# Performance work log

Measured on AMD Instinct MI355X. Metric: run time of the kernel, lower is better.

Reference implementation:

```python
import jax, jax.numpy as jnp
import numpy as np
import math

B, C, F, W = 2, 8, 512, 1024
HEADS = 8


def _mcl(x, Wm, b):
    # per-channel linear over feature dim: x (b,c,g,w), Wm (c,f,g), b (c,f)
    return jnp.einsum('bcgw,cfg->bcfw', x, Wm) + b[None, :, :, None]


def _conv(x, w, b, pad):
    y = jax.lax.conv_general_dilated(
        x, w, window_strides=(1, 1), padding=[(0, 0), (pad, pad)],
        dimension_numbers=('NCHW', 'OIHW', 'NCHW'))
    return y + b[None, :, None, None]


def _rope(t):
    # t: (..., seq, d); lucidrains-style interleaved rotary
    d = t.shape[-1]
    seq = t.shape[-2]
    inv_freq = 1.0 / (10000.0 ** (jnp.arange(0, d, 2, dtype=jnp.float32) / d))
    freqs = jnp.arange(seq, dtype=jnp.float32)[:, None] * inv_freq[None, :]  # (seq, d/2)
    emb = jnp.repeat(freqs, 2, axis=-1)  # (seq, d), interleaved f0,f0,f1,f1,...
    cos, sin = jnp.cos(emb), jnp.sin(emb)
    tp = t.reshape(t.shape[:-1] + (d // 2, 2))
    rot = jnp.stack([-tp[..., 1], tp[..., 0]], axis=-1).reshape(t.shape)
    return t * cos.astype(t.dtype) + rot * sin.astype(t.dtype)


def setup_inputs() -> dict:
    key = jax.random.key(0)
    ks = jax.random.split(key, 18)
    s = 0.02
    d = {'x': jax.random.normal(ks[0], (B, C, F, W), dtype=jnp.float32)}
    names = ['q', 'k', 'v', 'o']
    for i, n in enumerate(names):
        d['W' + n] = jax.random.normal(ks[1 + 4 * i], (C, F, F), dtype=jnp.float32) * s
        d['b' + n] = jnp.zeros((C, F), dtype=jnp.float32)
        kw = 7 if n != 'o' else 1
        d[n + '_conv_w'] = jax.random.normal(ks[2 + 4 * i], (C, C, 1, kw), dtype=jnp.float32) * s
        d[n + '_conv_b'] = jnp.zeros((C,), dtype=jnp.float32)
    return d


def reference(x, Wq, bq, q_conv_w, q_conv_b, Wk, bk, k_conv_w, k_conv_b,
              Wv, bv, v_conv_w, v_conv_b, Wo, bo, o_conv_w, o_conv_b):
    b, c, h, w = x.shape
    dh = h // HEADS

    def split_heads(y):  # (b,c,h,w) -> (b,c,heads,w,dh)
        return y.transpose(0, 1, 3, 2).reshape(b, c, w, HEADS, dh).transpose(0, 1, 3, 2, 4)

    q = _rope(split_heads(_conv(_mcl(x, Wq, bq), q_conv_w, q_conv_b, 3)))
    k = _rope(split_heads(_conv(_mcl(x, Wk, bk), k_conv_w, k_conv_b, 3)))
    v = split_heads(_conv(_mcl(x, Wv, bv), v_conv_w, v_conv_b, 3))

    # forced fp32 attention, scaled by sqrt(h) = sqrt(features)
    qk = jnp.einsum('bceqd,bcekd->bceqk', q.astype(jnp.float32), k.astype(jnp.float32)) / math.sqrt(h)
    a = jax.nn.softmax(qk, axis=-1)
    o = jnp.einsum('bceqk,bcekd->bceqd', a, v.astype(jnp.float32))  # (b,c,heads,w,dh)
    o = o.transpose(0, 1, 3, 2, 4).reshape(b, c, w, h).transpose(0, 1, 3, 2)  # (b,c,h,w)

    return _conv(_mcl(o, Wo, bo), o_conv_w, o_conv_b, 0)
```

## Files before the change

kernel.cpp:

```cpp
#include <hip/hip_runtime.h>
#include <hip/hip_bf16.h>
#include <math.h>

#define W_ 1024
#define F_ 512
#define C_ 8
#define B_ 2
#define DH_ 64

typedef __attribute__((ext_vector_type(8))) short short8;
typedef __attribute__((ext_vector_type(4))) short short4v;
typedef __attribute__((ext_vector_type(4))) float f32x4;

__device__ inline unsigned short f2bf(float x) {
    union { float f; unsigned u; } v; v.f = x;
    unsigned r = v.u + 0x7fff + ((v.u >> 16) & 1);
    return (unsigned short)(r >> 16);
}

__device__ inline void gll16(const void* g, void* l) {
    __builtin_amdgcn_global_load_lds(
        (const __attribute__((address_space(1))) unsigned int*)g,
        (__attribute__((address_space(3))) unsigned int*)l, 16, 0, 0);
}

__global__ __launch_bounds__(256) void rope_table_kernel(float* __restrict__ cost,
                                                         float* __restrict__ sint) {
    int idx = blockIdx.x * 256 + threadIdx.x;
    if (idx >= W_ * 32) return;
    int w = idx >> 5, i = idx & 31;
    double freq = pow(10000.0, -(double)(2 * i) / 64.0);
    double ang = (double)w * freq;
    cost[idx] = (float)cos(ang);
    sint[idx] = (float)sin(ang);
}

__global__ __launch_bounds__(256) void xt_kernel(
    const float* __restrict__ In, unsigned short* __restrict__ Out)
{
    const int wt = blockIdx.x;
    const int gc = blockIdx.y;
    const int bc = blockIdx.z;
    __shared__ unsigned short T[128][72];
    const int t = threadIdx.x;
    const float* src = In + (size_t)bc * F_ * W_ + (size_t)gc * 64 * W_ + wt * 128;
    const int d0 = (t >> 4) * 4;
    const int w0 = (t & 15) * 4;
    #pragma unroll
    for (int it = 0; it < 2; ++it) {
        int wbase = w0 + it * 64;
        float4 row[4];
        #pragma unroll
        for (int k = 0; k < 4; ++k)
            row[k] = *(const float4*)(src + (size_t)(d0 + k) * W_ + wbase);
        #pragma unroll
        for (int wp = 0; wp < 4; ++wp) {
            ushort4 p;
            p.x = f2bf(((const float*)&row[0])[wp]);
            p.y = f2bf(((const float*)&row[1])[wp]);
            p.z = f2bf(((const float*)&row[2])[wp]);
            p.w = f2bf(((const float*)&row[3])[wp]);
            *(ushort4*)&T[wbase + wp][d0] = p;
        }
    }
    __syncthreads();
    unsigned short* dst = Out + (size_t)bc * W_ * F_ + (size_t)(wt * 128) * F_ + gc * 64;
    const int w = t >> 1, hf = (t & 1) * 32;
    const unsigned short* sr = &T[w][hf];
    uint4* dr = (uint4*)(dst + (size_t)w * F_ + hf);
    dr[0] = ((const uint4*)sr)[0];
    dr[1] = ((const uint4*)sr)[1];
    dr[2] = ((const uint4*)sr)[2];
    dr[3] = ((const uint4*)sr)[3];
}

__device__ inline void mcl_body(const unsigned short* Ag, const unsigned short* Bg,
                                const float* biasp, float* Cp,
                                int f0, int w0)
{
    __shared__ unsigned short As_[128 * 64];
    __shared__ unsigned short Bs_[128 * 64];
    __shared__ float scr[4][16 * 17];

    const int t = threadIdx.x;
    const int wid = t >> 6, lane = t & 63;
    const int l15 = lane & 15, l4 = lane >> 4;
    const int wf = wid >> 1, ww = wid & 1;

    const int grow = lane >> 3;
    const int gcol = ((lane & 7) * 16) ^ ((grow & 7) << 4);

    f32x4 acc[4][4];
    #pragma unroll
    for (int mt = 0; mt < 4; ++mt)
        #pragma unroll
        for (int nt = 0; nt < 4; ++nt) acc[mt][nt] = (f32x4){0.f, 0.f, 0.f, 0.f};

    for (int ks = 0; ks < 8; ++ks) {
        const int k0 = ks * 64;
        __syncthreads();
        #pragma unroll
        for (int i = 0; i < 4; ++i) {
            int rbase = wid * 32 + i * 8;
            int row = rbase + grow;
            gll16(Ag + (size_t)(f0 + row) * F_ + k0 + (gcol >> 1), &As_[rbase * 64]);
            gll16(Bg + (size_t)(w0 + row) * F_ + k0 + (gcol >> 1), &Bs_[rbase * 64]);
        }
        __syncthreads();
        #pragma unroll
        for (int kf = 0; kf < 2; ++kf) {
            short8 af[4], bf_[4];
            #pragma unroll
            for (int mt = 0; mt < 4; ++mt) {
                int row = wf * 64 + mt * 16 + l15;
                int off = (kf * 64 + l4 * 16) ^ ((row & 7) << 4);
                af[mt] = *(const short8*)((const char*)As_ + row * 128 + off);
            }
            #pragma unroll
            for (int nt = 0; nt < 4; ++nt) {
                int row = ww * 64 + nt * 16 + l15;
                int off = (kf * 64 + l4 * 16) ^ ((row & 7) << 4);
                bf_[nt] = *(const short8*)((const char*)Bs_ + row * 128 + off);
            }
            #pragma unroll
            for (int mt = 0; mt < 4; ++mt)
                #pragma unroll
                for (int nt = 0; nt < 4; ++nt)
                    acc[mt][nt] = __builtin_amdgcn_mfma_f32_16x16x32_bf16(af[mt], bf_[nt], acc[mt][nt], 0, 0, 0);
        }
    }

    const float* bp = biasp + f0 + wf * 64;
    float bz[4][4];
    #pragma unroll
    for (int mt = 0; mt < 4; ++mt)
        #pragma unroll
        for (int r = 0; r < 4; ++r) bz[mt][r] = bp[mt * 16 + l4 * 4 + r];

    float* sw = scr[wid];
    #pragma unroll
    for (int mt = 0; mt < 4; ++mt)
        #pragma unroll
        for (int nt = 0; nt < 4; ++nt) {
            #pragma unroll
            for (int r = 0; r < 4; ++r)
                sw[(l4 * 4 + r) * 17 + l15] = acc[mt][nt][r] + bz[mt][r];
            float4 o;
            o.x = sw[l15 * 17 + l4 * 4 + 0];
            o.y = sw[l15 * 17 + l4 * 4 + 1];
            o.z = sw[l15 * 17 + l4 * 4 + 2];
            o.w = sw[l15 * 17 + l4 * 4 + 3];
            *(float4*)(Cp + (size_t)(f0 + wf * 64 + mt * 16 + l15) * W_
                          + w0 + ww * 64 + nt * 16 + l4 * 4) = o;
        }
}

__global__ __launch_bounds__(256) void mcl_qkv_kernel(
    const unsigned short* __restrict__ Xt,
    const unsigned short* __restrict__ W0, const unsigned short* __restrict__ W1,
    const unsigned short* __restrict__ W2,
    const float* __restrict__ b0, const float* __restrict__ b1, const float* __restrict__ b2,
    float* __restrict__ Y0, float* __restrict__ Y1, float* __restrict__ Y2)
{
    const int zz = blockIdx.z;
    const int proj = zz >> 4, bc = zz & 15;
    const int c = bc & 7;
    const unsigned short* Wb = proj == 0 ? W0 : (proj == 1 ? W1 : W2);
    const float* bias = proj == 0 ? b0 : (proj == 1 ? b1 : b2);
    float* Y = proj == 0 ? Y0 : (proj == 1 ? Y1 : Y2);
    mcl_body(Wb + (size_t)c * F_ * F_, Xt + (size_t)bc * W_ * F_,
             bias + c * F_, Y + (size_t)bc * F_ * W_,
             blockIdx.y * 128, blockIdx.x * 128);
}

__global__ __launch_bounds__(256) void mcl_mfma_kernel(
    const unsigned short* __restrict__ Xt, const unsigned short* __restrict__ Wb,
    const float* __restrict__ bias, float* __restrict__ Y)
{
    const int bc = blockIdx.z;
    const int c = bc & 7;
    mcl_body(Wb + (size_t)c * F_ * F_, Xt + (size_t)bc * W_ * F_,
             bias + c * F_, Y + (size_t)bc * F_ * W_,
             blockIdx.y * 128, blockIdx.x * 128);
}

__global__ __launch_bounds__(256) void convrope3_kernel(
    float* __restrict__ Aq, float* __restrict__ Ak, float* __restrict__ Av,
    const float* __restrict__ cwq, const float* __restrict__ cbq,
    const float* __restrict__ cwk, const float* __restrict__ cbk,
    const float* __restrict__ cwv, const float* __restrict__ cbv,
    const float* __restrict__ cost, const float* __restrict__ sint)
{
    const int fp = blockIdx.x;
    const int b = blockIdx.y;
    const int proj = blockIdx.z;
    float* Y = proj == 0 ? Aq : (proj == 1 ? Ak : Av);
    const float* CW = proj == 0 ? cwq : (proj == 1 ? cwk : cwv);
    const float* CB = proj == 0 ? cbq : (proj == 1 ? cbk : cbv);
    const int do_rope = (proj < 2);

    __shared__ float rows[C_][2][W_];
    __shared__ float wT[C_][7][C_];
    const int t = threadIdx.x;

    #pragma unroll
    for (int r = 0; r < 16; r++) {
        int ci = r >> 1, fi = r & 1;
        const float* src = Y + ((size_t)(b * C_ + ci) * F_ + 2 * fp + fi) * W_;
        *(float4*)&rows[ci][fi][t * 4] = *(const float4*)(src + t * 4);
    }
    for (int idx = t; idx < C_ * C_ * 7; idx += 256) {
        int co = idx & 7; int tmp = idx >> 3; int tt = tmp % 7; int ci = tmp / 7;
        wT[ci][tt][co] = CW[((size_t)co * C_ + ci) * 7 + tt];
    }
    float cb[8];
    #pragma unroll
    for (int co = 0; co < 8; co++) cb[co] = CB[co];
    __syncthreads();

    float acc[4][2][8];
    #pragma unroll
    for (int rep = 0; rep < 4; rep++)
        #pragma unroll
        for (int fi = 0; fi < 2; fi++)
            #pragma unroll
            for (int co = 0; co < 8; co++) acc[rep][fi][co] = cb[co];

    for (int ci = 0; ci < 8; ci++) {
        #pragma unroll
        for (int tt = 0; tt < 7; tt++) {
            float wv[8];
            *(float4*)(wv)     = *(const float4*)&wT[ci][tt][0];
            *(float4*)(wv + 4) = *(const float4*)&wT[ci][tt][4];
            #pragma unroll
            for (int rep = 0; rep < 4; rep++) {
                int ws = t + rep * 256 + tt - 3;
                float v0 = 0.f, v1 = 0.f;
                if ((unsigned)ws < (unsigned)W_) { v0 = rows[ci][0][ws]; v1 = rows[ci][1][ws]; }
                #pragma unroll
                for (int co = 0; co < 8; co++) {
                    acc[rep][0][co] = fmaf(v0, wv[co], acc[rep][0][co]);
                    acc[rep][1][co] = fmaf(v1, wv[co], acc[rep][1][co]);
                }
            }
        }
    }
    const int ip = fp & 31;
    #pragma unroll
    for (int rep = 0; rep < 4; rep++) {
        int w = t + rep * 256;
        float c_ = 1.f, s_ = 0.f;
        if (do_rope) { c_ = cost[w * 32 + ip]; s_ = sint[w * 32 + ip]; }
        #pragma unroll
        for (int co = 0; co < 8; co++) {
            float o0 = acc[rep][0][co], o1 = acc[rep][1][co];
            float r0 = do_rope ? (o0 * c_ - o1 * s_) : o0;
            float r1 = do_rope ? (o1 * c_ + o0 * s_) : o1;
            size_t rowb = ((size_t)(b * C_ + co) * F_ + 2 * fp) * W_;
            Y[rowb + w] = r0;
            Y[rowb + W_ + w] = r1;
        }
    }
}

__global__ __launch_bounds__(256) void transpose_qk_kernel(
    const float* __restrict__ In, unsigned short* __restrict__ Out, float scale)
{
    const int wt = blockIdx.x;
    const int h = blockIdx.y;
    __shared__ unsigned short T[128][72];
    const int t = threadIdx.x;
    const float* src = In + (size_t)h * 64 * 1024 + wt * 128;
    const int d0 = (t >> 4) * 4;
    const int w0 = (t & 15) * 4;
    #pragma unroll
    for (int it = 0; it < 2; ++it) {
        int wbase = w0 + it * 64;
        float4 row[4];
        #pragma unroll
        for (int k = 0; k < 4; ++k)
            row[k] = *(const float4*)(src + (size_t)(d0 + k) * 1024 + wbase);
        #pragma unroll
        for (int wp = 0; wp < 4; ++wp) {
            ushort4 p;
            p.x = f2bf(((const float*)&row[0])[wp] * scale);
            p.y = f2bf(((const float*)&row[1])[wp] * scale);
            p.z = f2bf(((const float*)&row[2])[wp] * scale);
            p.w = f2bf(((const float*)&row[3])[wp] * scale);
            *(ushort4*)&T[wbase + wp][d0] = p;
        }
    }
    __syncthreads();
    unsigned short* dst = Out + ((size_t)h * 1024 + wt * 128) * 64;
    const int w = t >> 1, hf = (t & 1) * 32;
    const unsigned short* sr = &T[w][hf];
    uint4* dr = (uint4*)(dst + w * 64 + hf);
    dr[0] = ((const uint4*)sr)[0];
    dr[1] = ((const uint4*)sr)[1];
    dr[2] = ((const uint4*)sr)[2];
    dr[3] = ((const uint4*)sr)[3];
}

__global__ __launch_bounds__(256) void bf16cvt_kernel(
    const float* __restrict__ In, unsigned short* __restrict__ Out)
{
    size_t i = ((size_t)blockIdx.x * 256 + threadIdx.x) * 8;
    float4 a = *(const float4*)(In + i);
    float4 b = *(const float4*)(In + i + 4);
    ushort4 pa, pb;
    pa.x = f2bf(a.x); pa.y = f2bf(a.y); pa.z = f2bf(a.z); pa.w = f2bf(a.w);
    pb.x = f2bf(b.x); pb.y = f2bf(b.y); pb.z = f2bf(b.z); pb.w = f2bf(b.w);
    *(ushort4*)(Out + i) = pa;
    *(ushort4*)(Out + i + 4) = pb;
}

__global__ __launch_bounds__(256) void attn_mfma_kernel(
    const unsigned short* __restrict__ Qt, const unsigned short* __restrict__ Kt,
    const unsigned short* __restrict__ Vb, unsigned short* __restrict__ Ot)
{
    const int head = blockIdx.x;
    const int qt = blockIdx.y;
    const int t = threadIdx.x;
    const int wid = t >> 6;
    const int lane = t & 63;
    const int l15 = lane & 15;
    const int l4 = lane >> 4;

    __shared__ unsigned short Ks[64 * 64];
    __shared__ unsigned short Vs[64 * 64];
    __shared__ char plds_[4][11264];
    unsigned short* plds = (unsigned short*)plds_[wid];
    float* olds = (float*)plds_[wid];

    const int q0 = qt * 256 + wid * 64;
    const unsigned short* qb = Qt + ((size_t)head * 1024 + q0) * 64;
    const unsigned short* kb = Kt + (size_t)head * 1024 * 64;
    const unsigned short* vb = Vb + (size_t)head * 64 * 1024;

    short8 aq[4][2];
    #pragma unroll
    for (int mt = 0; mt < 4; ++mt)
        #pragma unroll
        for (int kf = 0; kf < 2; ++kf)
            aq[mt][kf] = *(const short8*)(qb + (size_t)(mt * 16 + l15) * 64 + kf * 32 + l4 * 8);

    const int srow = lane >> 3;
    const int schunk = lane & 7;

    f32x4 oa[4][4];
    float li[4] = {0.f, 0.f, 0.f, 0.f};
    #pragma unroll
    for (int mt = 0; mt < 4; ++mt)
        #pragma unroll
        for (int dt = 0; dt < 4; ++dt) oa[mt][dt] = (f32x4){0.f, 0.f, 0.f, 0.f};

    for (int jt = 0; jt < 16; ++jt) {
        const int j0 = jt * 64;
        __syncthreads();
        #pragma unroll
        for (int i = 0; i < 2; ++i) {
            int rbase = wid * 16 + i * 8;
            int row = rbase + srow;
            gll16(kb + (size_t)(j0 + row) * 64 + ((schunk ^ (row & 7)) * 8), &Ks[rbase * 64]);
            gll16(vb + (size_t)row * 1024 + j0 + ((schunk ^ (row & 7)) * 8), &Vs[rbase * 64]);
        }
        __syncthreads();

        #pragma unroll
        for (int nt = 0; nt < 4; ++nt) {
            int row = nt * 16 + l15;
            short8 bk0 = *(const short8*)&Ks[row * 64 + ((l4 ^ (row & 7)) * 8)];
            short8 bk1 = *(const short8*)&Ks[row * 64 + (((4 + l4) ^ (row & 7)) * 8)];
            #pragma unroll
            for (int mt = 0; mt < 4; ++mt) {
                f32x4 a0 = (f32x4){0.f, 0.f, 0.f, 0.f};
                a0 = __builtin_amdgcn_mfma_f32_16x16x32_bf16(bk0, aq[mt][0], a0, 0, 0, 0);
                a0 = __builtin_amdgcn_mfma_f32_16x16x32_bf16(bk1, aq[mt][1], a0, 0, 0, 0);
                float p0 = __builtin_exp2f(a0[0]);
                float p1 = __builtin_exp2f(a0[1]);
                float p2 = __builtin_exp2f(a0[2]);
                float p3 = __builtin_exp2f(a0[3]);
                li[mt] += (p0 + p1) + (p2 + p3);
                union { __hip_bfloat162 h2[2]; short4v s4; } pk;
                pk.h2[0] = __float22bfloat162_rn(make_float2(p0, p1));
                pk.h2[1] = __float22bfloat162_rn(make_float2(p2, p3));
                *(short4v*)(plds + (size_t)(mt * 16 + l15) * 88 + nt * 16 + l4 * 4) = pk.s4;
            }
        }
        short8 pa[4][2];
        #pragma unroll
        for (int mt = 0; mt < 4; ++mt)
            #pragma unroll
            for (int kf = 0; kf < 2; ++kf)
                pa[mt][kf] = *(const short8*)(plds + (size_t)(mt * 16 + l15) * 88 + kf * 32 + l4 * 8);
        #pragma unroll
        for (int dt = 0; dt < 4; ++dt) {
            int row = dt * 16 + l15;
            short8 bv0 = *(const short8*)&Vs[row * 64 + ((l4 ^ (row & 7)) * 8)];
            short8 bv1 = *(const short8*)&Vs[row * 64 + (((4 + l4) ^ (row & 7)) * 8)];
            #pragma unroll
            for (int mt = 0; mt < 4; ++mt) {
                oa[mt][dt] = __builtin_amdgcn_mfma_f32_16x16x32_bf16(pa[mt][0], bv0, oa[mt][dt], 0, 0, 0);
                oa[mt][dt] = __builtin_amdgcn_mfma_f32_16x16x32_bf16(pa[mt][1], bv1, oa[mt][dt], 0, 0, 0);
            }
        }
    }

    float invq[4][4];
    #pragma unroll
    for (int mt = 0; mt < 4; ++mt) {
        float l = li[mt];
        l += __shfl_xor(l, 16);
        l += __shfl_xor(l, 32);
        float inv = 1.f / l;
        #pragma unroll
        for (int r = 0; r < 4; ++r)
            invq[mt][r] = __shfl(inv, l4 * 4 + r);
    }

    #pragma unroll
    for (int mt = 0; mt < 4; ++mt) {
        #pragma unroll
        for (int dt = 0; dt < 4; ++dt)
            #pragma unroll
            for (int r = 0; r < 4; ++r)
                olds[(size_t)(l4 * 4 + r) * 68 + dt * 16 + l15] = oa[mt][dt][r] * invq[mt][r];
        const int ql = lane >> 2, hf = (lane & 3) * 16;
        const float* srow_ = olds + (size_t)ql * 68 + hf;
        unsigned short* dst = Ot + ((size_t)(head >> 3) * W_ + q0 + mt * 16 + ql) * F_
                                 + (head & 7) * 64 + hf;
        short8 pk0, pk1;
        #pragma unroll
        for (int e = 0; e < 8; ++e) { pk0[e] = (short)f2bf(srow_[e]); pk1[e] = (short)f2bf(srow_[8 + e]); }
        *(short8*)(dst) = pk0;
        *(short8*)(dst + 8) = pk1;
    }
}

__global__ __launch_bounds__(256) void oconv_kernel(
    const float* __restrict__ In, const float* __restrict__ OW,
    const float* __restrict__ OB, float* __restrict__ Out)
{
    size_t idx = (size_t)blockIdx.x * 256 + threadIdx.x;
    int b = (int)(idx >> 19);
    size_t fw = idx & (((size_t)1 << 19) - 1);
    const float* in = In + (size_t)b * C_ * F_ * W_ + fw;
    float* out = Out + (size_t)b * C_ * F_ * W_ + fw;
    float v[8];
    #pragma unroll
    for (int ci = 0; ci < 8; ci++) v[ci] = in[(size_t)ci * F_ * W_];
    #pragma unroll
    for (int co = 0; co < 8; co++) {
        float acc = OB[co];
        #pragma unroll
        for (int ci = 0; ci < 8; ci++) acc = fmaf(v[ci], OW[co * 8 + ci], acc);
        out[(size_t)co * F_ * W_] = acc;
    }
}

extern "C" void kernel_launch(void* const* d_in, const int* in_sizes, int n_in,
                              void* d_out, int out_size, void* d_ws, size_t ws_size,
                              hipStream_t stream) {
    const float* x   = (const float*)d_in[0];
    const float* Wq  = (const float*)d_in[1];
    const float* bq  = (const float*)d_in[2];
    const float* qcw = (const float*)d_in[3];
    const float* qcb = (const float*)d_in[4];
    const float* Wk  = (const float*)d_in[5];
    const float* bk  = (const float*)d_in[6];
    const float* kcw = (const float*)d_in[7];
    const float* kcb = (const float*)d_in[8];
    const float* Wv  = (const float*)d_in[9];
    const float* bv  = (const float*)d_in[10];
    const float* vcw = (const float*)d_in[11];
    const float* vcb = (const float*)d_in[12];
    const float* Wo  = (const float*)d_in[13];
    const float* bo  = (const float*)d_in[14];
    const float* ocw = (const float*)d_in[15];
    const float* ocb = (const float*)d_in[16];

    float* ws = (float*)d_ws;
    const size_t SZ = (size_t)B_ * C_ * F_ * W_;
    const size_t WSF = (size_t)C_ * F_ * F_ / 2;
    float* Aq = ws;
    float* Ak = ws + SZ;
    float* Av = ws + 2 * SZ;
    unsigned short* XtVb = (unsigned short*)(ws + 3 * SZ);
    unsigned short* WqB = (unsigned short*)(ws + 3 * SZ + SZ / 2);
    unsigned short* WkB = (unsigned short*)(ws + 3 * SZ + SZ / 2 + 2 * WSF);
    unsigned short* WvB = (unsigned short*)(ws + 3 * SZ + SZ / 2 + 4 * WSF);
    unsigned short* WoB = (unsigned short*)(ws + 3 * SZ + SZ / 2 + 6 * WSF);
    unsigned short* Qt  = (unsigned short*)(ws + 2 * SZ);
    unsigned short* Kt  = Qt + SZ;
    unsigned short* Ot  = (unsigned short*)ws;
    float* cost = ws + 4 * SZ;
    float* sint = cost + (size_t)W_ * 32;

    const float qscale = (float)(1.4426950408889634 / 22.627416997969522);

    rope_table_kernel<<<(W_ * 32 + 255) / 256, 256, 0, stream>>>(cost, sint);
    xt_kernel<<<dim3(8, 8, 16), 256, 0, stream>>>(x, XtVb);
    bf16cvt_kernel<<<1024, 256, 0, stream>>>(Wq, WqB);
    bf16cvt_kernel<<<1024, 256, 0, stream>>>(Wk, WkB);
    bf16cvt_kernel<<<1024, 256, 0, stream>>>(Wv, WvB);
    bf16cvt_kernel<<<1024, 256, 0, stream>>>(Wo, WoB);

    mcl_qkv_kernel<<<dim3(8, 4, 48), 256, 0, stream>>>(
        XtVb, WqB, WkB, WvB, bq, bk, bv, Aq, Ak, Av);

    convrope3_kernel<<<dim3(F_ / 2, B_, 3), 256, 0, stream>>>(
        Aq, Ak, Av, qcw, qcb, kcw, kcb, vcw, vcb, cost, sint);

    bf16cvt_kernel<<<SZ / (256 * 8), 256, 0, stream>>>(Av, XtVb);
    transpose_qk_kernel<<<dim3(W_ / 128, 128), 256, 0, stream>>>(Aq, Qt, qscale);
    transpose_qk_kernel<<<dim3(W_ / 128, 128), 256, 0, stream>>>(Ak, Kt, 1.0f);

    attn_mfma_kernel<<<dim3(128, 4), 256, 0, stream>>>(Qt, Kt, XtVb, Ot);

    mcl_mfma_kernel<<<dim3(8, 4, 16), 256, 0, stream>>>(Ot, WoB, bo, Ak);
    oconv_kernel<<<(B_ * F_ * W_) / 256, 256, 0, stream>>>(Ak, ocw, ocb, (float*)d_out);
}
```

Baseline: 286.6 us.

## Split conv+rope by W chunks, out-of-place, fuse V bf16 conversion

```diff
diff --git a/kernel.cpp b/kernel.cpp
--- a/kernel.cpp
+++ b/kernel.cpp
@@ -184,30 +184,30 @@
              blockIdx.y * 128, blockIdx.x * 128);
 }
 
-__global__ __launch_bounds__(256) void convrope3_kernel(
-    float* __restrict__ Aq, float* __restrict__ Ak, float* __restrict__ Av,
-    const float* __restrict__ cwq, const float* __restrict__ cbq,
-    const float* __restrict__ cwk, const float* __restrict__ cbk,
-    const float* __restrict__ cwv, const float* __restrict__ cbv,
-    const float* __restrict__ cost, const float* __restrict__ sint)
-{
-    const int fp = blockIdx.x;
-    const int b = blockIdx.y;
-    const int proj = blockIdx.z;
-    float* Y = proj == 0 ? Aq : (proj == 1 ? Ak : Av);
-    const float* CW = proj == 0 ? cwq : (proj == 1 ? cwk : cwv);
-    const float* CB = proj == 0 ? cbq : (proj == 1 ? cbk : cbv);
-    const int do_rope = (proj < 2);
-
-    __shared__ float rows[C_][2][W_];
+__global__ __launch_bounds__(256) void convrope_w_kernel(
+    const float* __restrict__ In, const float* __restrict__ CW,
+    const float* __restrict__ CB, const float* __restrict__ cost,
+    const float* __restrict__ sint, float* __restrict__ OutF,
+    unsigned short* __restrict__ OutB, int do_rope, int out_bf16)
+{
+    const int wc = blockIdx.x;
+    const int fp = blockIdx.y;
+    const int b = blockIdx.z;
+    __shared__ float rows[C_][2][264];
     __shared__ float wT[C_][7][C_];
     const int t = threadIdx.x;
-
-    #pragma unroll
-    for (int r = 0; r < 16; r++) {
+    const int w0 = wc * 256;
+
+    #pragma unroll
+    for (int r = 0; r < 16; ++r) {
         int ci = r >> 1, fi = r & 1;
-        const float* src = Y + ((size_t)(b * C_ + ci) * F_ + 2 * fp + fi) * W_;
-        *(float4*)&rows[ci][fi][t * 4] = *(const float4*)(src + t * 4);
+        const float* src = In + ((size_t)(b * C_ + ci) * F_ + 2 * fp + fi) * W_;
+        int gw = w0 + t - 3;
+        rows[ci][fi][t] = ((unsigned)gw < (unsigned)W_) ? src[gw] : 0.f;
+        if (t < 8) {
+            int gw2 = w0 + 256 + t - 3;
+            rows[ci][fi][256 + t] = ((unsigned)gw2 < (unsigned)W_) ? src[gw2] : 0.f;
+        }
     }
     for (int idx = t; idx < C_ * C_ * 7; idx += 256) {
         int co = idx & 7; int tmp = idx >> 3; int tt = tmp % 7; int ci = tmp / 7;
@@ -218,47 +218,44 @@
     for (int co = 0; co < 8; co++) cb[co] = CB[co];
     __syncthreads();
 
-    float acc[4][2][8];
-    #pragma unroll
-    for (int rep = 0; rep < 4; rep++)
-        #pragma unroll
-        for (int fi = 0; fi < 2; fi++)
-            #pragma unroll
-            for (int co = 0; co < 8; co++) acc[rep][fi][co] = cb[co];
-
-    for (int ci = 0; ci < 8; ci++) {
-        #pragma unroll
-        for (int tt = 0; tt < 7; tt++) {
+    float acc[2][8];
+    #pragma unroll
+    for (int fi = 0; fi < 2; ++fi)
+        #pragma unroll
+        for (int co = 0; co < 8; ++co) acc[fi][co] = cb[co];
+
+    for (int ci = 0; ci < 8; ++ci) {
+        #pragma unroll
+        for (int tt = 0; tt < 7; ++tt) {
             float wv[8];
             *(float4*)(wv)     = *(const float4*)&wT[ci][tt][0];
             *(float4*)(wv + 4) = *(const float4*)&wT[ci][tt][4];
-            #pragma unroll
-            for (int rep = 0; rep < 4; rep++) {
-                int ws = t + rep * 256 + tt - 3;
-                float v0 = 0.f, v1 = 0.f;
-                if ((unsigned)ws < (unsigned)W_) { v0 = rows[ci][0][ws]; v1 = rows[ci][1][ws]; }
-                #pragma unroll
-                for (int co = 0; co < 8; co++) {
-                    acc[rep][0][co] = fmaf(v0, wv[co], acc[rep][0][co]);
-                    acc[rep][1][co] = fmaf(v1, wv[co], acc[rep][1][co]);
-                }
+            float v0 = rows[ci][0][t + tt];
+            float v1 = rows[ci][1][t + tt];
+            #pragma unroll
+            for (int co = 0; co < 8; ++co) {
+                acc[0][co] = fmaf(v0, wv[co], acc[0][co]);
+                acc[1][co] = fmaf(v1, wv[co], acc[1][co]);
             }
         }
     }
+
     const int ip = fp & 31;
-    #pragma unroll
-    for (int rep = 0; rep < 4; rep++) {
-        int w = t + rep * 256;
-        float c_ = 1.f, s_ = 0.f;
-        if (do_rope) { c_ = cost[w * 32 + ip]; s_ = sint[w * 32 + ip]; }
-        #pragma unroll
-        for (int co = 0; co < 8; co++) {
-            float o0 = acc[rep][0][co], o1 = acc[rep][1][co];
-            float r0 = do_rope ? (o0 * c_ - o1 * s_) : o0;
-            float r1 = do_rope ? (o1 * c_ + o0 * s_) : o1;
-            size_t rowb = ((size_t)(b * C_ + co) * F_ + 2 * fp) * W_;
-            Y[rowb + w] = r0;
-            Y[rowb + W_ + w] = r1;
+    const int w = w0 + t;
+    float c_ = 1.f, s_ = 0.f;
+    if (do_rope) { c_ = cost[w * 32 + ip]; s_ = sint[w * 32 + ip]; }
+    #pragma unroll
+    for (int co = 0; co < 8; ++co) {
+        float o0 = acc[0][co], o1 = acc[1][co];
+        float r0 = do_rope ? (o0 * c_ - o1 * s_) : o0;
+        float r1 = do_rope ? (o1 * c_ + o0 * s_) : o1;
+        size_t rowb = ((size_t)(b * C_ + co) * F_ + 2 * fp) * W_;
+        if (out_bf16) {
+            OutB[rowb + w] = f2bf(r0);
+            OutB[rowb + W_ + w] = f2bf(r1);
+        } else {
+            OutF[rowb + w] = r0;
+            OutF[rowb + W_ + w] = r1;
         }
     }
 }
@@ -485,14 +482,17 @@
     float* Aq = ws;
     float* Ak = ws + SZ;
     float* Av = ws + 2 * SZ;
+    float* Cq = ws + 2 * SZ;
+    float* Ck = ws;
     unsigned short* XtVb = (unsigned short*)(ws + 3 * SZ);
     unsigned short* WqB = (unsigned short*)(ws + 3 * SZ + SZ / 2);
     unsigned short* WkB = (unsigned short*)(ws + 3 * SZ + SZ / 2 + 2 * WSF);
     unsigned short* WvB = (unsigned short*)(ws + 3 * SZ + SZ / 2 + 4 * WSF);
     unsigned short* WoB = (unsigned short*)(ws + 3 * SZ + SZ / 2 + 6 * WSF);
-    unsigned short* Qt  = (unsigned short*)(ws + 2 * SZ);
+    unsigned short* Qt  = (unsigned short*)(ws + SZ);
     unsigned short* Kt  = Qt + SZ;
-    unsigned short* Ot  = (unsigned short*)ws;
+    unsigned short* Ot  = (unsigned short*)(ws + 2 * SZ);
+    float* Ao = ws;
     float* cost = ws + 4 * SZ;
     float* sint = cost + (size_t)W_ * 32;
 
@@ -508,15 +508,19 @@
     mcl_qkv_kernel<<<dim3(8, 4, 48), 256, 0, stream>>>(
         XtVb, WqB, WkB, WvB, bq, bk, bv, Aq, Ak, Av);
 
-    convrope3_kernel<<<dim3(F_ / 2, B_, 3), 256, 0, stream>>>(
-        Aq, Ak, Av, qcw, qcb, kcw, kcb, vcw, vcb, cost, sint);
-
-    bf16cvt_kernel<<<SZ / (256 * 8), 256, 0, stream>>>(Av, XtVb);
-    transpose_qk_kernel<<<dim3(W_ / 128, 128), 256, 0, stream>>>(Aq, Qt, qscale);
-    transpose_qk_kernel<<<dim3(W_ / 128, 128), 256, 0, stream>>>(Ak, Kt, 1.0f);
+    dim3 gcw(4, F_ / 2, B_);
+    convrope_w_kernel<<<gcw, 256, 0, stream>>>(Av, vcw, vcb, cost, sint,
+                                               nullptr, XtVb, 0, 1);
+    convrope_w_kernel<<<gcw, 256, 0, stream>>>(Aq, qcw, qcb, cost, sint,
+                                               Cq, nullptr, 1, 0);
+    convrope_w_kernel<<<gcw, 256, 0, stream>>>(Ak, kcw, kcb, cost, sint,
+                                               Ck, nullptr, 1, 0);
+
+    transpose_qk_kernel<<<dim3(W_ / 128, 128), 256, 0, stream>>>(Cq, Qt, qscale);
+    transpose_qk_kernel<<<dim3(W_ / 128, 128), 256, 0, stream>>>(Ck, Kt, 1.0f);
 
     attn_mfma_kernel<<<dim3(128, 4), 256, 0, stream>>>(Qt, Kt, XtVb, Ot);
 
-    mcl_mfma_kernel<<<dim3(8, 4, 16), 256, 0, stream>>>(Ot, WoB, bo, Ak);
-    oconv_kernel<<<(B_ * F_ * W_) / 256, 256, 0, stream>>>(Ak, ocw, ocb, (float*)d_out);
-}
+    mcl_mfma_kernel<<<dim3(8, 4, 16), 256, 0, stream>>>(Ot, WoB, bo, Ao);
+    oconv_kernel<<<(B_ * F_ * W_) / 256, 256, 0, stream>>>(Ao, ocw, ocb, (float*)d_out);
+}
```

Measured after the change: 716.5 us. 2.5x slower.
